# Kernel tuning notes

Measured on AMD Instinct MI355X. Metric: run time of the kernel, lower is better.

Reference implementation:

```python
import jax, jax.numpy as jnp
import numpy as np

B, H, W, C = 32, 64, 64, 256
WS, SS = 8, 4            # window_size, shift_size
HEADS, HD = C // 32, 32  # heads, head_dim
SCALE = HD ** -0.5
WS2 = WS * WS
NW = (H // WS) * (W // WS)  # windows per image


def _rel_pos_indices(ws):
    # matches ShiftedWindowAttention.get_indices
    x = np.arange(ws)
    y1, x1, y2, x2 = np.meshgrid(x, x, x, x, indexing='ij')
    idx = (y1 - y2 + ws - 1) * (2 * ws - 1) + (x1 - x2 + ws - 1)
    return jnp.asarray(idx.reshape(-1), dtype=jnp.int32)  # (ws^4,)


def _shift_mask(h, w, ws, ss):
    # standard Swin shifted-window mask: True where attention is forbidden
    img = np.zeros((h, w), np.int32)
    cnt = 0
    for hs in (slice(0, -ws), slice(-ws, -ss), slice(-ss, None)):
        for wsl in (slice(0, -ws), slice(-ws, -ss), slice(-ss, None)):
            img[hs, wsl] = cnt
            cnt += 1
    win = img.reshape(h // ws, ws, w // ws, ws).transpose(0, 2, 1, 3).reshape(-1, ws * ws)
    return jnp.asarray(win[:, :, None] != win[:, None, :])  # (nW, ws^2, ws^2)


REL_IDX = _rel_pos_indices(WS)
MASK = _shift_mask(H, W, WS, SS)


def setup_inputs() -> dict:
    key = jax.random.key(0)
    ks = jax.random.split(key, 6)
    s = C ** -0.5
    return {
        'x': jax.random.normal(ks[0], (B, H * W, C), jnp.float32),
        'w_qkv': jax.random.normal(ks[1], (C, 3 * C), jnp.float32) * s,
        'b_qkv': jnp.zeros((3 * C,), jnp.float32),
        'w_out': jax.random.normal(ks[2], (C, C), jnp.float32) * s,
        'b_out': jnp.zeros((C,), jnp.float32),
        'pos_enc': jax.random.normal(ks[3], (HEADS, (2 * WS - 1) ** 2), jnp.float32) * 0.02,
    }


def reference(x, w_qkv, b_qkv, w_out, b_out, pos_enc):
    b = x.shape[0]
    xi = x.reshape(b, H, W, C)
    xi = jnp.roll(xi, (-SS, -SS), axis=(1, 2))  # cyclic shift
    nh, nw = H // WS, W // WS
    # window partition -> (b*nW, ws^2, C)
    xw = xi.reshape(b, nh, WS, nw, WS, C).transpose(0, 1, 3, 2, 4, 5).reshape(b * NW, WS2, C)
    qkv = xw @ w_qkv + b_qkv
    q, k, v = jnp.split(qkv, 3, axis=-1)
    split = lambda t: t.reshape(b * NW, WS2, HEADS, HD).transpose(0, 2, 1, 3)
    q, k, v = split(q), split(k), split(v)  # (b*nW, heads, ws^2, hd)
    attn = jnp.einsum('whqd,whkd->whqk', q, k) * SCALE
    bias = pos_enc[:, REL_IDX].reshape(HEADS, WS2, WS2)
    attn = attn + bias[None]
    # shifted-window mask per window position
    attn = attn.reshape(b, NW, HEADS, WS2, WS2)
    attn = jnp.where(MASK[None, :, None], -jnp.inf, attn)
    attn = jax.nn.softmax(attn.reshape(b * NW, HEADS, WS2, WS2), axis=-1)
    out = jnp.einsum('whqk,whkd->whqd', attn, v)
    out = out.transpose(0, 2, 1, 3).reshape(b * NW, WS2, C)
    out = out @ w_out + b_out
    # reverse window partition
    out = out.reshape(b, nh, nw, WS, WS, C).transpose(0, 1, 3, 2, 4, 5).reshape(b, H, W, C)
    out = jnp.roll(out, (SS, SS), axis=(1, 2))  # reverse cyclic shift
    return out.reshape(b, H * W, C)
```

## Files before the change

kernel.cpp:

```cpp
#include <hip/hip_runtime.h>

typedef unsigned short ushort_t;
typedef __bf16 bf16x8 __attribute__((ext_vector_type(8)));
typedef float f32x4 __attribute__((ext_vector_type(4)));
typedef unsigned short u16x4 __attribute__((ext_vector_type(4)));

#define SCALE_F 0.17677669529663687f
#define SWZ3(row) (((row) & 3) << 4)
#define SWZ7(row) (((row) & 7) << 4)

__device__ __forceinline__ ushort_t f2bf(float f) {
  union { float f; unsigned u; } v; v.f = f;
  unsigned u = v.u;
  return (ushort_t)((u + 0x7FFFu + ((u >> 16) & 1u)) >> 16);
}
__device__ __forceinline__ float bf2f(ushort_t b) {
  union { unsigned u; float f; } v; v.u = ((unsigned)b) << 16;
  return v.f;
}
__device__ __forceinline__ void fence_lds() {
  asm volatile("s_waitcnt lgkmcnt(0)" ::: "memory");
  __builtin_amdgcn_sched_barrier(0);
}

__global__ __launch_bounds__(256, 1) void prep_weights(
    const float* __restrict__ wqkv, const float* __restrict__ wout,
    ushort_t* __restrict__ wqkvT, ushort_t* __restrict__ woutT) {
  int i = blockIdx.x * 256 + threadIdx.x;
  if (i < 768 * 256) {
    int n = i >> 8, k = i & 255;
    wqkvT[i] = f2bf(wqkv[k * 768 + n]);
  } else {
    int j = i - 768 * 256;
    int n = j >> 8, k = j & 255;
    woutT[j] = f2bf(wout[k * 256 + n]);
  }
}

__global__ __launch_bounds__(256, 1) void prep_bias(
    const float* __restrict__ pos_enc, ushort_t* __restrict__ biasB) {
  int i = blockIdx.x * 256 + threadIdx.x;
  int h = i >> 12, q = (i >> 6) & 63, k = i & 63;
  int y1 = q >> 3, x1 = q & 7, y2 = k >> 3, x2 = k & 7;
  biasB[i] = f2bf(pos_enc[h * 225 + (y1 - y2 + 7) * 15 + (x1 - x2 + 7)]);
}

__global__ __launch_bounds__(256, 2) void swin_attn(
    const float* __restrict__ x,
    const float* __restrict__ b_qkv,
    const float* __restrict__ b_out,
    const ushort_t* __restrict__ wqkvT,
    const ushort_t* __restrict__ woutT,
    const ushort_t* __restrict__ biasB,
    float* __restrict__ out) {
  __shared__ __attribute__((aligned(16))) char smem[81920];

  const int tid  = threadIdx.x;
  const int wid  = blockIdx.x;
  const int bb   = wid >> 6;
  const int w64  = wid & 63;
  const int wy   = w64 >> 3, wx = w64 & 7;
  const int wave = tid >> 6, lane = tid & 63;
  const int g    = lane >> 4, cc = lane & 15;
  const bool maskY = (wy == 7), maskX = (wx == 7);
  const bool masked = maskY || maskX;

  {
    const float* xb = x + (size_t)bb * 4096 * 256;
    #pragma unroll
    for (int it = 0; it < 16; ++it) {
      int fi = tid + 256 * it;
      int r = fi >> 6, c4 = fi & 63;
      int hh = (8 * wy + (r >> 3) + 4) & 63;
      int ww = (8 * wx + (r & 7) + 4) & 63;
      const float4 v = ((const float4*)(xb + ((size_t)hh * 64 + ww) * 256))[c4];
      uint2 pk;
      pk.x = (unsigned)f2bf(v.x) | ((unsigned)f2bf(v.y) << 16);
      pk.y = (unsigned)f2bf(v.z) | ((unsigned)f2bf(v.w) << 16);
      *(uint2*)(smem + r * 512 + ((8 * c4) ^ SWZ7(r))) = pk;
    }
  }
  __syncthreads();

  char* slab = smem + 32768 + wave * 12288;
  f32x4 oacc0[2][4], oacc1[2][4];
  float rinv0[4], rinv1[4];

  auto qkv = [&](int h) {
    f32x4 aq[2][4], ak[2][4], av[2][4];
    #pragma unroll
    for (int c = 0; c < 2; ++c)
      #pragma unroll
      for (int t = 0; t < 4; ++t) {
        aq[c][t] = (f32x4){0.f,0.f,0.f,0.f};
        ak[c][t] = (f32x4){0.f,0.f,0.f,0.f};
        av[c][t] = (f32x4){0.f,0.f,0.f,0.f};
      }
    const ushort_t* wq = wqkvT + (size_t)(      32 * h) * 256;
    const ushort_t* wk = wqkvT + (size_t)(256 + 32 * h) * 256;
    const ushort_t* wv = wqkvT + (size_t)(512 + 32 * h) * 256;
    #pragma unroll
    for (int ks = 0; ks < 8; ++ks) {
      bf16x8 aks[4];
      #pragma unroll
      for (int t = 0; t < 4; ++t) {
        int row = 16 * t + cc;
        aks[t] = *(const bf16x8*)(smem + row * 512 + ((64 * ks + 16 * g) ^ SWZ7(row)));
      }
      #pragma unroll
      for (int c = 0; c < 2; ++c) {
        int roff = (16 * c + cc) * 256 + 32 * ks + 8 * g;
        bf16x8 fq = *(const bf16x8*)&wq[roff];
        bf16x8 fk = *(const bf16x8*)&wk[roff];
        bf16x8 fv = *(const bf16x8*)&wv[roff];
        #pragma unroll
        for (int t = 0; t < 4; ++t) {
          aq[c][t] = __builtin_amdgcn_mfma_f32_16x16x32_bf16(fq, aks[t], aq[c][t], 0, 0, 0);
          ak[c][t] = __builtin_amdgcn_mfma_f32_16x16x32_bf16(fk, aks[t], ak[c][t], 0, 0, 0);
          av[c][t] = __builtin_amdgcn_mfma_f32_16x16x32_bf16(aks[t], fv, av[c][t], 0, 0, 0);
        }
      }
    }
    fence_lds();
    #pragma unroll
    for (int c = 0; c < 2; ++c) {
      float4 bq4 = *(const float4*)&b_qkv[      32 * h + 16 * c + 4 * g];
      float4 bk4 = *(const float4*)&b_qkv[256 + 32 * h + 16 * c + 4 * g];
      float bqa[4] = {bq4.x, bq4.y, bq4.z, bq4.w};
      float bka[4] = {bk4.x, bk4.y, bk4.z, bk4.w};
      #pragma unroll
      for (int t = 0; t < 4; ++t) {
        int tok = 16 * t + cc;
        u16x4 pq, pk;
        #pragma unroll
        for (int i = 0; i < 4; ++i) {
          pq[i] = f2bf((aq[c][t][i] + bqa[i]) * SCALE_F);
          pk[i] = f2bf(ak[c][t][i] + bka[i]);
        }
        *(u16x4*)(slab +        tok * 64 + ((32 * c + 8 * g) ^ SWZ3(tok))) = pq;
        *(u16x4*)(slab + 4096 + tok * 64 + ((32 * c + 8 * g) ^ SWZ3(tok))) = pk;
      }
      float bv = b_qkv[512 + 32 * h + 16 * c + cc];
      int ch = 16 * c + cc;
      #pragma unroll
      for (int t = 0; t < 4; ++t) {
        u16x4 pv;
        #pragma unroll
        for (int i = 0; i < 4; ++i) pv[i] = f2bf(av[c][t][i] + bv);
        *(u16x4*)(slab + 8192 + ch * 128 + ((32 * t + 8 * g) ^ SWZ7(ch))) = pv;
      }
    }
    fence_lds();
  };

  auto attn = [&](int h, f32x4 (*oacc)[4], float* rinv) {
    bf16x8 qf[4], kf[4], vf[2][2];
    #pragma unroll
    for (int t = 0; t < 4; ++t) {
      int row = 16 * t + cc;
      qf[t] = *(const bf16x8*)(slab +        row * 64 + ((16 * g) ^ SWZ3(row)));
      kf[t] = *(const bf16x8*)(slab + 4096 + row * 64 + ((16 * g) ^ SWZ3(row)));
    }
    #pragma unroll
    for (int c = 0; c < 2; ++c) {
      int ch = 16 * c + cc;
      #pragma unroll
      for (int ks = 0; ks < 2; ++ks)
        vf[c][ks] = *(const bf16x8*)(slab + 8192 + ch * 128 + ((64 * ks + 16 * g) ^ SWZ7(ch)));
    }
    fence_lds();

    f32x4 sacc[4][4];
    #pragma unroll
    for (int nt = 0; nt < 4; ++nt)
      #pragma unroll
      for (int qt = 0; qt < 4; ++qt) sacc[nt][qt] = (f32x4){0.f,0.f,0.f,0.f};
    #pragma unroll
    for (int qt = 0; qt < 4; ++qt)
      #pragma unroll
      for (int nt = 0; nt < 4; ++nt)
        sacc[nt][qt] = __builtin_amdgcn_mfma_f32_16x16x32_bf16(kf[nt], qf[qt], sacc[nt][qt], 0, 0, 0);

    const ushort_t* bh = biasB + h * 4096;
    const int rxq = maskX ? (((cc & 7) < 4) ? 1 : 2) : 0;
    #pragma unroll
    for (int qt = 0; qt < 4; ++qt) {
      int q = 16 * qt + cc;
      float sv[4][4];
      float mx = -3.0e38f;
      #pragma unroll
      for (int nt = 0; nt < 4; ++nt) {
        u16x4 b4 = *(const u16x4*)&bh[q * 64 + 16 * nt + 4 * g];
        #pragma unroll
        for (int i = 0; i < 4; ++i)
          sv[nt][i] = sacc[nt][qt][i] + bf2f(b4[i]);
      }
      if (masked) {
        int qy = q >> 3;
        int lq = (maskY ? ((qy < 4) ? 1 : 2) : 0) * 3 + rxq;
        #pragma unroll
        for (int nt = 0; nt < 4; ++nt)
          #pragma unroll
          for (int i = 0; i < 4; ++i) {
            int k  = 16 * nt + 4 * g + i;
            int lk = (maskY ? (((k >> 3) < 4) ? 1 : 2) : 0) * 3 +
                     (maskX ? (((k & 7) < 4) ? 1 : 2) : 0);
            if (lq != lk) sv[nt][i] = -3.0e38f;
          }
      }
      #pragma unroll
      for (int nt = 0; nt < 4; ++nt)
        #pragma unroll
        for (int i = 0; i < 4; ++i) mx = fmaxf(mx, sv[nt][i]);
      mx = fmaxf(mx, __shfl_xor(mx, 16));
      mx = fmaxf(mx, __shfl_xor(mx, 32));
      float sum = 0.f;
      #pragma unroll
      for (int nt = 0; nt < 4; ++nt)
        #pragma unroll
        for (int i = 0; i < 4; ++i) {
          float e = __expf(sv[nt][i] - mx);
          sv[nt][i] = e;
          sum += e;
        }
      sum += __shfl_xor(sum, 16);
      sum += __shfl_xor(sum, 32);
      rinv[qt] = 1.0f / sum;
      #pragma unroll
      for (int nt = 0; nt < 4; ++nt) {
        u16x4 pp;
        #pragma unroll
        for (int i = 0; i < 4; ++i) pp[i] = f2bf(sv[nt][i]);
        *(u16x4*)(slab + q * 128 + ((32 * nt + 8 * g) ^ SWZ7(q))) = pp;
      }
    }
    fence_lds();

    bf16x8 pf[4][2];
    #pragma unroll
    for (int qt = 0; qt < 4; ++qt) {
      int q = 16 * qt + cc;
      #pragma unroll
      for (int ks = 0; ks < 2; ++ks)
        pf[qt][ks] = *(const bf16x8*)(slab + q * 128 + ((64 * ks + 16 * g) ^ SWZ7(q)));
    }
    #pragma unroll
    for (int c = 0; c < 2; ++c)
      #pragma unroll
      for (int qt = 0; qt < 4; ++qt) oacc[c][qt] = (f32x4){0.f,0.f,0.f,0.f};
    #pragma unroll
    for (int ks = 0; ks < 2; ++ks)
      #pragma unroll
      for (int c = 0; c < 2; ++c)
        #pragma unroll
        for (int qt = 0; qt < 4; ++qt)
          oacc[c][qt] = __builtin_amdgcn_mfma_f32_16x16x32_bf16(vf[c][ks], pf[qt][ks], oacc[c][qt], 0, 0, 0);
  };

  auto writeO = [&](f32x4 (*oacc)[4], float* rinv, int hh) {
    #pragma unroll
    for (int c = 0; c < 2; ++c)
      #pragma unroll
      for (int qt = 0; qt < 4; ++qt) {
        int q = 16 * qt + cc;
        u16x4 po;
        #pragma unroll
        for (int i = 0; i < 4; ++i) po[i] = f2bf(oacc[c][qt][i] * rinv[qt]);
        int cb = 2 * (64 * wave + 32 * hh + 16 * c + 4 * g);
        *(u16x4*)(smem + q * 512 + (cb ^ SWZ7(q))) = po;
      }
  };

  qkv(2 * wave);
  attn(2 * wave, oacc0, rinv0);
  qkv(2 * wave + 1);
  __syncthreads();
  writeO(oacc0, rinv0, 0);
  attn(2 * wave + 1, oacc1, rinv1);
  writeO(oacc1, rinv1, 1);
  __syncthreads();

  {
    f32x4 pacc[4][4];
    #pragma unroll
    for (int c = 0; c < 4; ++c)
      #pragma unroll
      for (int t = 0; t < 4; ++t) pacc[c][t] = (f32x4){0.f,0.f,0.f,0.f};
    #pragma unroll
    for (int ks = 0; ks < 8; ++ks) {
      bf16x8 of[4];
      #pragma unroll
      for (int t = 0; t < 4; ++t) {
        int row = 16 * t + cc;
        of[t] = *(const bf16x8*)(smem + row * 512 + ((64 * ks + 16 * g) ^ SWZ7(row)));
      }
      #pragma unroll
      for (int c = 0; c < 4; ++c) {
        bf16x8 wf = *(const bf16x8*)&woutT[(size_t)(64 * wave + 16 * c + cc) * 256 + 32 * ks + 8 * g];
        #pragma unroll
        for (int t = 0; t < 4; ++t)
          pacc[c][t] = __builtin_amdgcn_mfma_f32_16x16x32_bf16(wf, of[t], pacc[c][t], 0, 0, 0);
      }
    }
    #pragma unroll
    for (int c = 0; c < 4; ++c) {
      int ch = 64 * wave + 16 * c + 4 * g;
      float4 bo4 = *(const float4*)&b_out[ch];
      #pragma unroll
      for (int t = 0; t < 4; ++t) {
        int q = 16 * t + cc;
        int hh2 = (8 * wy + (q >> 3) + 4) & 63;
        int ww2 = (8 * wx + (q & 7) + 4) & 63;
        float4 st;
        st.x = pacc[c][t][0] + bo4.x;
        st.y = pacc[c][t][1] + bo4.y;
        st.z = pacc[c][t][2] + bo4.z;
        st.w = pacc[c][t][3] + bo4.w;
        *(float4*)&out[(((size_t)bb * 4096) + hh2 * 64 + ww2) * 256 + ch] = st;
      }
    }
  }
}

extern "C" void kernel_launch(void* const* d_in, const int* in_sizes, int n_in,
                              void* d_out, int out_size, void* d_ws, size_t ws_size,
                              hipStream_t stream) {
  const float* x       = (const float*)d_in[0];
  const float* w_qkv   = (const float*)d_in[1];
  const float* b_qkv   = (const float*)d_in[2];
  const float* w_out   = (const float*)d_in[3];
  const float* b_out   = (const float*)d_in[4];
  const float* pos_enc = (const float*)d_in[5];
  float* out = (float*)d_out;

  ushort_t* wqkvT = (ushort_t*)d_ws;
  ushort_t* woutT = wqkvT + 768 * 256;
  ushort_t* biasB = woutT + 256 * 256;

  prep_weights<<<dim3((768 * 256 + 256 * 256) / 256), dim3(256), 0, stream>>>(
      w_qkv, w_out, wqkvT, woutT);
  prep_bias<<<dim3(128), dim3(256), 0, stream>>>(pos_enc, biasB);
  swin_attn<<<dim3(2048), dim3(256), 0, stream>>>(
      x, b_qkv, b_out, wqkvT, woutT, biasB, out);
}
```

Baseline: 204.7 us.

## Keep Q/K/V and softmax probabilities in registers via permuted MFMA layouts

Measured after the change: 188.7 us. 7.8% less time.

```diff
diff --git a/kernel.cpp b/kernel.cpp
--- a/kernel.cpp
+++ b/kernel.cpp
@@ -1,59 +1,65 @@
 #include <hip/hip_runtime.h>
 
-typedef unsigned short ushort_t;
+typedef __bf16 bf16_t;
+typedef __bf16 bf16x4 __attribute__((ext_vector_type(4)));
 typedef __bf16 bf16x8 __attribute__((ext_vector_type(8)));
 typedef float f32x4 __attribute__((ext_vector_type(4)));
-typedef unsigned short u16x4 __attribute__((ext_vector_type(4)));
-
-#define SCALE_F 0.17677669529663687f
-#define SWZ3(row) (((row) & 3) << 4)
-#define SWZ7(row) (((row) & 7) << 4)
-
-__device__ __forceinline__ ushort_t f2bf(float f) {
-  union { float f; unsigned u; } v; v.f = f;
-  unsigned u = v.u;
-  return (ushort_t)((u + 0x7FFFu + ((u >> 16) & 1u)) >> 16);
-}
-__device__ __forceinline__ float bf2f(ushort_t b) {
-  union { unsigned u; float f; } v; v.u = ((unsigned)b) << 16;
-  return v.f;
-}
-__device__ __forceinline__ void fence_lds() {
-  asm volatile("s_waitcnt lgkmcnt(0)" ::: "memory");
-  __builtin_amdgcn_sched_barrier(0);
+
+#define SCALE_LOG2E 0.25510803519787995f
+#define LOG2E 1.4426950408889634f
+#define SWZ(row) (((row) & 15) << 4)
+
+__device__ __forceinline__ f32x4 mk4(float4 v) { return (f32x4){v.x, v.y, v.z, v.w}; }
+__device__ __forceinline__ bf16x8 pack2(f32x4 a, f32x4 b) {
+  bf16x4 lo = __builtin_convertvector(a, bf16x4);
+  bf16x4 hi = __builtin_convertvector(b, bf16x4);
+  return __builtin_shufflevector(lo, hi, 0, 1, 2, 3, 4, 5, 6, 7);
 }
 
 __global__ __launch_bounds__(256, 1) void prep_weights(
     const float* __restrict__ wqkv, const float* __restrict__ wout,
-    ushort_t* __restrict__ wqkvT, ushort_t* __restrict__ woutT) {
+    bf16_t* __restrict__ wqkvT, bf16_t* __restrict__ woutT) {
   int i = blockIdx.x * 256 + threadIdx.x;
-  if (i < 768 * 256) {
-    int n = i >> 8, k = i & 255;
-    wqkvT[i] = f2bf(wqkv[k * 768 + n]);
+  int n = i >> 8, k = i & 255;
+  if (n < 768) {
+    int s = n >> 8, hl = n & 255;
+    int src;
+    if (s < 2) {
+      int h = hl >> 5, w = hl & 31, c = (w >> 4) & 1, r = w & 15;
+      src = 32 * h + 8 * (r >> 2) + 4 * c + (r & 3);
+    } else {
+      src = hl;
+    }
+    float v = wqkv[k * 768 + s * 256 + src];
+    if (s == 0) v *= SCALE_LOG2E;
+    wqkvT[n * 256 + k] = (bf16_t)v;
   } else {
-    int j = i - 768 * 256;
-    int n = j >> 8, k = j & 255;
-    woutT[j] = f2bf(wout[k * 256 + n]);
+    int m = n - 768;
+    woutT[m * 256 + k] = (bf16_t)wout[k * 256 + m];
   }
 }
 
 __global__ __launch_bounds__(256, 1) void prep_bias(
-    const float* __restrict__ pos_enc, ushort_t* __restrict__ biasB) {
+    const float* __restrict__ pos_enc, bf16_t* __restrict__ biasI) {
   int i = blockIdx.x * 256 + threadIdx.x;
-  int h = i >> 12, q = (i >> 6) & 63, k = i & 63;
-  int y1 = q >> 3, x1 = q & 7, y2 = k >> 3, x2 = k & 7;
-  biasB[i] = f2bf(pos_enc[h * 225 + (y1 - y2 + 7) * 15 + (x1 - x2 + 7)]);
+  int ii = i & 3, lane = (i >> 2) & 63, nt = (i >> 8) & 3, qt = (i >> 10) & 3, h = i >> 12;
+  int g = lane >> 4, cc = lane & 15;
+  int q = 32 * (qt >> 1) + 4 * (qt & 1) + 8 * (cc >> 2) + (cc & 3);
+  int key = 32 * (nt >> 1) + 4 * (nt & 1) + 8 * g + ii;
+  int qy = q >> 3, qx = q & 7, ky = key >> 3, kx = key & 7;
+  biasI[i] = (bf16_t)(pos_enc[h * 225 + (qy - ky + 7) * 15 + (qx - kx + 7)] * LOG2E);
 }
 
 __global__ __launch_bounds__(256, 2) void swin_attn(
     const float* __restrict__ x,
     const float* __restrict__ b_qkv,
     const float* __restrict__ b_out,
-    const ushort_t* __restrict__ wqkvT,
-    const ushort_t* __restrict__ woutT,
-    const ushort_t* __restrict__ biasB,
+    const bf16_t* __restrict__ wqkvT,
+    const bf16_t* __restrict__ woutT,
+    const bf16_t* __restrict__ biasI,
     float* __restrict__ out) {
-  __shared__ __attribute__((aligned(16))) char smem[81920];
+  __shared__ __attribute__((aligned(16))) char smem[65536];
+  char* Osm = smem + 32768;
 
   const int tid  = threadIdx.x;
   const int wid  = blockIdx.x;
@@ -63,7 +69,7 @@
   const int wave = tid >> 6, lane = tid & 63;
   const int g    = lane >> 4, cc = lane & 15;
   const bool maskY = (wy == 7), maskX = (wx == 7);
-  const bool masked = maskY || maskX;
+  const int rb = 8 * (cc >> 2) + (cc & 3);
 
   {
     const float* xb = x + (size_t)bb * 4096 * 256;
@@ -74,140 +80,99 @@
       int hh = (8 * wy + (r >> 3) + 4) & 63;
       int ww = (8 * wx + (r & 7) + 4) & 63;
       const float4 v = ((const float4*)(xb + ((size_t)hh * 64 + ww) * 256))[c4];
-      uint2 pk;
-      pk.x = (unsigned)f2bf(v.x) | ((unsigned)f2bf(v.y) << 16);
-      pk.y = (unsigned)f2bf(v.z) | ((unsigned)f2bf(v.w) << 16);
-      *(uint2*)(smem + r * 512 + ((8 * c4) ^ SWZ7(r))) = pk;
+      bf16x4 pk = __builtin_convertvector(mk4(v), bf16x4);
+      *(bf16x4*)(smem + r * 512 + ((8 * c4) ^ SWZ(r))) = pk;
     }
   }
   __syncthreads();
 
-  char* slab = smem + 32768 + wave * 12288;
-  f32x4 oacc0[2][4], oacc1[2][4];
-  float rinv0[4], rinv1[4];
-
-  auto qkv = [&](int h) {
-    f32x4 aq[2][4], ak[2][4], av[2][4];
+  #pragma unroll
+  for (int hh = 0; hh < 2; ++hh) {
+    const int h = 2 * wave + hh;
+
+    f32x4 aq[2][4], ak[2][4], av[4][2];
     #pragma unroll
     for (int c = 0; c < 2; ++c)
       #pragma unroll
       for (int t = 0; t < 4; ++t) {
-        aq[c][t] = (f32x4){0.f,0.f,0.f,0.f};
-        ak[c][t] = (f32x4){0.f,0.f,0.f,0.f};
-        av[c][t] = (f32x4){0.f,0.f,0.f,0.f};
-      }
-    const ushort_t* wq = wqkvT + (size_t)(      32 * h) * 256;
-    const ushort_t* wk = wqkvT + (size_t)(256 + 32 * h) * 256;
-    const ushort_t* wv = wqkvT + (size_t)(512 + 32 * h) * 256;
+        aq[c][t] = (f32x4){0.f, 0.f, 0.f, 0.f};
+        ak[c][t] = (f32x4){0.f, 0.f, 0.f, 0.f};
+        av[t][c] = (f32x4){0.f, 0.f, 0.f, 0.f};
+      }
+    const bf16_t* wq = wqkvT + (size_t)(      32 * h) * 256;
+    const bf16_t* wk = wqkvT + (size_t)(256 + 32 * h) * 256;
+    const bf16_t* wv = wqkvT + (size_t)(512 + 32 * h) * 256;
     #pragma unroll
     for (int ks = 0; ks < 8; ++ks) {
       bf16x8 aks[4];
       #pragma unroll
       for (int t = 0; t < 4; ++t) {
-        int row = 16 * t + cc;
-        aks[t] = *(const bf16x8*)(smem + row * 512 + ((64 * ks + 16 * g) ^ SWZ7(row)));
+        int row = 32 * (t >> 1) + 4 * (t & 1) + rb;
+        aks[t] = *(const bf16x8*)(smem + row * 512 + ((64 * ks + 16 * g) ^ SWZ(row)));
       }
       #pragma unroll
       for (int c = 0; c < 2; ++c) {
-        int roff = (16 * c + cc) * 256 + 32 * ks + 8 * g;
-        bf16x8 fq = *(const bf16x8*)&wq[roff];
-        bf16x8 fk = *(const bf16x8*)&wk[roff];
-        bf16x8 fv = *(const bf16x8*)&wv[roff];
+        int ro = (16 * c + cc) * 256 + 32 * ks + 8 * g;
+        bf16x8 fq = *(const bf16x8*)&wq[ro];
+        bf16x8 fk = *(const bf16x8*)&wk[ro];
+        bf16x8 fv = *(const bf16x8*)&wv[ro];
         #pragma unroll
         for (int t = 0; t < 4; ++t) {
           aq[c][t] = __builtin_amdgcn_mfma_f32_16x16x32_bf16(fq, aks[t], aq[c][t], 0, 0, 0);
           ak[c][t] = __builtin_amdgcn_mfma_f32_16x16x32_bf16(fk, aks[t], ak[c][t], 0, 0, 0);
-          av[c][t] = __builtin_amdgcn_mfma_f32_16x16x32_bf16(aks[t], fv, av[c][t], 0, 0, 0);
+          av[t][c] = __builtin_amdgcn_mfma_f32_16x16x32_bf16(aks[t], fv, av[t][c], 0, 0, 0);
         }
       }
     }
-    fence_lds();
-    #pragma unroll
-    for (int c = 0; c < 2; ++c) {
-      float4 bq4 = *(const float4*)&b_qkv[      32 * h + 16 * c + 4 * g];
-      float4 bk4 = *(const float4*)&b_qkv[256 + 32 * h + 16 * c + 4 * g];
-      float bqa[4] = {bq4.x, bq4.y, bq4.z, bq4.w};
-      float bka[4] = {bk4.x, bk4.y, bk4.z, bk4.w};
-      #pragma unroll
-      for (int t = 0; t < 4; ++t) {
-        int tok = 16 * t + cc;
-        u16x4 pq, pk;
-        #pragma unroll
-        for (int i = 0; i < 4; ++i) {
-          pq[i] = f2bf((aq[c][t][i] + bqa[i]) * SCALE_F);
-          pk[i] = f2bf(ak[c][t][i] + bka[i]);
+
+    bf16x8 qp[4], kp[4], vp[2][2];
+    {
+      f32x4 bq0 = mk4(*(const float4*)&b_qkv[32 * h + 8 * g]) * SCALE_LOG2E;
+      f32x4 bq1 = mk4(*(const float4*)&b_qkv[32 * h + 8 * g + 4]) * SCALE_LOG2E;
+      f32x4 bk0 = mk4(*(const float4*)&b_qkv[256 + 32 * h + 8 * g]);
+      f32x4 bk1 = mk4(*(const float4*)&b_qkv[256 + 32 * h + 8 * g + 4]);
+      #pragma unroll
+      for (int t = 0; t < 4; ++t) {
+        qp[t] = pack2(aq[0][t] + bq0, aq[1][t] + bq1);
+        kp[t] = pack2(ak[0][t] + bk0, ak[1][t] + bk1);
+      }
+      #pragma unroll
+      for (int c = 0; c < 2; ++c) {
+        float bv = b_qkv[512 + 32 * h + 16 * c + cc];
+        f32x4 bv4 = (f32x4){bv, bv, bv, bv};
+        #pragma unroll
+        for (int ks = 0; ks < 2; ++ks)
+          vp[c][ks] = pack2(av[2 * ks][c] + bv4, av[2 * ks + 1][c] + bv4);
+      }
+    }
+
+    f32x4 sacc[4][4];
+    #pragma unroll
+    for (int nt = 0; nt < 4; ++nt)
+      #pragma unroll
+      for (int qt = 0; qt < 4; ++qt) sacc[nt][qt] = (f32x4){0.f, 0.f, 0.f, 0.f};
+    #pragma unroll
+    for (int qt = 0; qt < 4; ++qt)
+      #pragma unroll
+      for (int nt = 0; nt < 4; ++nt)
+        sacc[nt][qt] = __builtin_amdgcn_mfma_f32_16x16x32_bf16(kp[nt], qp[qt], sacc[nt][qt], 0, 0, 0);
+
+    bf16x8 pf[4][2];
+    const bf16_t* bI = biasI + h * 4096 + lane * 4;
+    #pragma unroll
+    for (int qt = 0; qt < 4; ++qt) {
+      f32x4 sv[4];
+      #pragma unroll
+      for (int nt = 0; nt < 4; ++nt) {
+        bool dead = (maskY && ((qt < 2) != (nt < 2))) || (maskX && ((qt & 1) != (nt & 1)));
+        if (dead) {
+          sv[nt] = (f32x4){-3.0e38f, -3.0e38f, -3.0e38f, -3.0e38f};
+        } else {
+          bf16x4 bb = *(const bf16x4*)&bI[(qt * 4 + nt) * 256];
+          sv[nt] = sacc[nt][qt] + __builtin_convertvector(bb, f32x4);
         }
-        *(u16x4*)(slab +        tok * 64 + ((32 * c + 8 * g) ^ SWZ3(tok))) = pq;
-        *(u16x4*)(slab + 4096 + tok * 64 + ((32 * c + 8 * g) ^ SWZ3(tok))) = pk;
-      }
-      float bv = b_qkv[512 + 32 * h + 16 * c + cc];
-      int ch = 16 * c + cc;
-      #pragma unroll
-      for (int t = 0; t < 4; ++t) {
-        u16x4 pv;
-        #pragma unroll
-        for (int i = 0; i < 4; ++i) pv[i] = f2bf(av[c][t][i] + bv);
-        *(u16x4*)(slab + 8192 + ch * 128 + ((32 * t + 8 * g) ^ SWZ7(ch))) = pv;
-      }
-    }
-    fence_lds();
-  };
-
-  auto attn = [&](int h, f32x4 (*oacc)[4], float* rinv) {
-    bf16x8 qf[4], kf[4], vf[2][2];
-    #pragma unroll
-    for (int t = 0; t < 4; ++t) {
-      int row = 16 * t + cc;
-      qf[t] = *(const bf16x8*)(slab +        row * 64 + ((16 * g) ^ SWZ3(row)));
-      kf[t] = *(const bf16x8*)(slab + 4096 + row * 64 + ((16 * g) ^ SWZ3(row)));
-    }
-    #pragma unroll
-    for (int c = 0; c < 2; ++c) {
-      int ch = 16 * c + cc;
-      #pragma unroll
-      for (int ks = 0; ks < 2; ++ks)
-        vf[c][ks] = *(const bf16x8*)(slab + 8192 + ch * 128 + ((64 * ks + 16 * g) ^ SWZ7(ch)));
-    }
-    fence_lds();
-
-    f32x4 sacc[4][4];
-    #pragma unroll
-    for (int nt = 0; nt < 4; ++nt)
-      #pragma unroll
-      for (int qt = 0; qt < 4; ++qt) sacc[nt][qt] = (f32x4){0.f,0.f,0.f,0.f};
-    #pragma unroll
-    for (int qt = 0; qt < 4; ++qt)
-      #pragma unroll
-      for (int nt = 0; nt < 4; ++nt)
-        sacc[nt][qt] = __builtin_amdgcn_mfma_f32_16x16x32_bf16(kf[nt], qf[qt], sacc[nt][qt], 0, 0, 0);
-
-    const ushort_t* bh = biasB + h * 4096;
-    const int rxq = maskX ? (((cc & 7) < 4) ? 1 : 2) : 0;
-    #pragma unroll
-    for (int qt = 0; qt < 4; ++qt) {
-      int q = 16 * qt + cc;
-      float sv[4][4];
+      }
       float mx = -3.0e38f;
-      #pragma unroll
-      for (int nt = 0; nt < 4; ++nt) {
-        u16x4 b4 = *(const u16x4*)&bh[q * 64 + 16 * nt + 4 * g];
-        #pragma unroll
-        for (int i = 0; i < 4; ++i)
-          sv[nt][i] = sacc[nt][qt][i] + bf2f(b4[i]);
-      }
-      if (masked) {
-        int qy = q >> 3;
-        int lq = (maskY ? ((qy < 4) ? 1 : 2) : 0) * 3 + rxq;
-        #pragma unroll
-        for (int nt = 0; nt < 4; ++nt)
-          #pragma unroll
-          for (int i = 0; i < 4; ++i) {
-            int k  = 16 * nt + 4 * g + i;
-            int lk = (maskY ? (((k >> 3) < 4) ? 1 : 2) : 0) * 3 +
-                     (maskX ? (((k & 7) < 4) ? 1 : 2) : 0);
-            if (lq != lk) sv[nt][i] = -3.0e38f;
-          }
-      }
       #pragma unroll
       for (int nt = 0; nt < 4; ++nt)
         #pragma unroll
@@ -219,65 +184,42 @@
       for (int nt = 0; nt < 4; ++nt)
         #pragma unroll
         for (int i = 0; i < 4; ++i) {
-          float e = __expf(sv[nt][i] - mx);
+          float e = exp2f(sv[nt][i] - mx);
           sv[nt][i] = e;
           sum += e;
         }
       sum += __shfl_xor(sum, 16);
       sum += __shfl_xor(sum, 32);
-      rinv[qt] = 1.0f / sum;
-      #pragma unroll
-      for (int nt = 0; nt < 4; ++nt) {
-        u16x4 pp;
-        #pragma unroll
-        for (int i = 0; i < 4; ++i) pp[i] = f2bf(sv[nt][i]);
-        *(u16x4*)(slab + q * 128 + ((32 * nt + 8 * g) ^ SWZ7(q))) = pp;
-      }
-    }
-    fence_lds();
-
-    bf16x8 pf[4][2];
-    #pragma unroll
-    for (int qt = 0; qt < 4; ++qt) {
-      int q = 16 * qt + cc;
-      #pragma unroll
-      for (int ks = 0; ks < 2; ++ks)
-        pf[qt][ks] = *(const bf16x8*)(slab + q * 128 + ((64 * ks + 16 * g) ^ SWZ7(q)));
-    }
+      float rinv = 1.0f / sum;
+      #pragma unroll
+      for (int nt = 0; nt < 4; ++nt) sv[nt] *= rinv;
+      pf[qt][0] = pack2(sv[0], sv[1]);
+      pf[qt][1] = pack2(sv[2], sv[3]);
+    }
+
+    f32x4 oacc[2][4];
     #pragma unroll
     for (int c = 0; c < 2; ++c)
       #pragma unroll
-      for (int qt = 0; qt < 4; ++qt) oacc[c][qt] = (f32x4){0.f,0.f,0.f,0.f};
+      for (int qt = 0; qt < 4; ++qt) oacc[c][qt] = (f32x4){0.f, 0.f, 0.f, 0.f};
     #pragma unroll
     for (int ks = 0; ks < 2; ++ks)
       #pragma unroll
       for (int c = 0; c < 2; ++c)
         #pragma unroll
         for (int qt = 0; qt < 4; ++qt)
-          oacc[c][qt] = __builtin_amdgcn_mfma_f32_16x16x32_bf16(vf[c][ks], pf[qt][ks], oacc[c][qt], 0, 0, 0);
-  };
-
-  auto writeO = [&](f32x4 (*oacc)[4], float* rinv, int hh) {
+          oacc[c][qt] = __builtin_amdgcn_mfma_f32_16x16x32_bf16(vp[c][ks], pf[qt][ks], oacc[c][qt], 0, 0, 0);
+
     #pragma unroll
     for (int c = 0; c < 2; ++c)
       #pragma unroll
       for (int qt = 0; qt < 4; ++qt) {
-        int q = 16 * qt + cc;
-        u16x4 po;
-        #pragma unroll
-        for (int i = 0; i < 4; ++i) po[i] = f2bf(oacc[c][qt][i] * rinv[qt]);
-        int cb = 2 * (64 * wave + 32 * hh + 16 * c + 4 * g);
-        *(u16x4*)(smem + q * 512 + (cb ^ SWZ7(q))) = po;
-      }
-  };
-
-  qkv(2 * wave);
-  attn(2 * wave, oacc0, rinv0);
-  qkv(2 * wave + 1);
-  __syncthreads();
-  writeO(oacc0, rinv0, 0);
-  attn(2 * wave + 1, oacc1, rinv1);
-  writeO(oacc1, rinv1, 1);
+        int tok = 32 * (qt >> 1) + 4 * (qt & 1) + rb;
+        bf16x4 ob = __builtin_convertvector(oacc[c][qt], bf16x4);
+        *(bf16x4*)(Osm + tok * 512 +
+                   ((2 * (64 * wave + 32 * hh + 16 * c + 4 * g)) ^ SWZ(tok))) = ob;
+      }
+  }
   __syncthreads();
 
   {
@@ -285,26 +227,26 @@
     #pragma unroll
     for (int c = 0; c < 4; ++c)
       #pragma unroll
-      for (int t = 0; t < 4; ++t) pacc[c][t] = (f32x4){0.f,0.f,0.f,0.f};
+      for (int t = 0; t < 4; ++t) pacc[c][t] = (f32x4){0.f, 0.f, 0.f, 0.f};
     #pragma unroll
     for (int ks = 0; ks < 8; ++ks) {
       bf16x8 of[4];
       #pragma unroll
       for (int t = 0; t < 4; ++t) {
         int row = 16 * t + cc;
-        of[t] = *(const bf16x8*)(smem + row * 512 + ((64 * ks + 16 * g) ^ SWZ7(row)));
-      }
-      #pragma unroll
-      for (int c = 0; c < 4; ++c) {
-        bf16x8 wf = *(const bf16x8*)&woutT[(size_t)(64 * wave + 16 * c + cc) * 256 + 32 * ks + 8 * g];
+        of[t] = *(const bf16x8*)(Osm + row * 512 + ((64 * ks + 16 * g) ^ SWZ(row)));
+      }
+      #pragma unroll
+      for (int c2 = 0; c2 < 4; ++c2) {
+        bf16x8 wf = *(const bf16x8*)&woutT[(size_t)(64 * wave + 16 * c2 + cc) * 256 + 32 * ks + 8 * g];
         #pragma unroll
         for (int t = 0; t < 4; ++t)
-          pacc[c][t] = __builtin_amdgcn_mfma_f32_16x16x32_bf16(wf, of[t], pacc[c][t], 0, 0, 0);
-      }
-    }
-    #pragma unroll
-    for (int c = 0; c < 4; ++c) {
-      int ch = 64 * wave + 16 * c + 4 * g;
+          pacc[c2][t] = __builtin_amdgcn_mfma_f32_16x16x32_bf16(wf, of[t], pacc[c2][t], 0, 0, 0);
+      }
+    }
+    #pragma unroll
+    for (int c2 = 0; c2 < 4; ++c2) {
+      int ch = 64 * wave + 16 * c2 + 4 * g;
       float4 bo4 = *(const float4*)&b_out[ch];
       #pragma unroll
       for (int t = 0; t < 4; ++t) {
@@ -312,10 +254,10 @@
         int hh2 = (8 * wy + (q >> 3) + 4) & 63;
         int ww2 = (8 * wx + (q & 7) + 4) & 63;
         float4 st;
-        st.x = pacc[c][t][0] + bo4.x;
-        st.y = pacc[c][t][1] + bo4.y;
-        st.z = pacc[c][t][2] + bo4.z;
-        st.w = pacc[c][t][3] + bo4.w;
+        st.x = pacc[c2][t][0] + bo4.x;
+        st.y = pacc[c2][t][1] + bo4.y;
+        st.z = pacc[c2][t][2] + bo4.z;
+        st.w = pacc[c2][t][3] + bo4.w;
         *(float4*)&out[(((size_t)bb * 4096) + hh2 * 64 + ww2) * 256 + ch] = st;
       }
     }
@@ -333,13 +275,12 @@
   const float* pos_enc = (const float*)d_in[5];
   float* out = (float*)d_out;
 
-  ushort_t* wqkvT = (ushort_t*)d_ws;
-  ushort_t* woutT = wqkvT + 768 * 256;
-  ushort_t* biasB = woutT + 256 * 256;
-
-  prep_weights<<<dim3((768 * 256 + 256 * 256) / 256), dim3(256), 0, stream>>>(
-      w_qkv, w_out, wqkvT, woutT);
-  prep_bias<<<dim3(128), dim3(256), 0, stream>>>(pos_enc, biasB);
+  bf16_t* wqkvT = (bf16_t*)d_ws;
+  bf16_t* woutT = wqkvT + 768 * 256;
+  bf16_t* biasI = woutT + 256 * 256;
+
+  prep_weights<<<dim3(1024), dim3(256), 0, stream>>>(w_qkv, w_out, wqkvT, woutT);
+  prep_bias<<<dim3(128), dim3(256), 0, stream>>>(pos_enc, biasI);
   swin_attn<<<dim3(2048), dim3(256), 0, stream>>>(
-      x, b_qkv, b_out, wqkvT, woutT, biasB, out);
-}
+      x, b_qkv, b_out, wqkvT, woutT, biasI, out);
+}
```
